# Kernel optimization log

Measured on AMD Instinct MI355X. Metric: run time of the kernel, lower is better.

The kernel has to match this reference:

```python
import jax, jax.numpy as jnp
import numpy as np

SEQ_LEN = 8192
D_MODEL = 1024
D_K = 128
D_V = 128


def setup_inputs() -> dict:
    key = jax.random.key(0)
    kx, kq, kk, kv = jax.random.split(key, 4)
    # xavier-uniform scale for (out, in) linear weights
    def xavier(k, out_f, in_f):
        lim = np.sqrt(6.0 / (in_f + out_f))
        return jax.random.uniform(k, (out_f, in_f), jnp.float32, -lim, lim)
    return {
        "X": jax.random.normal(kx, (SEQ_LEN, D_MODEL), jnp.float32),
        "Wq": xavier(kq, D_K, D_MODEL),
        "Wk": xavier(kk, D_K, D_MODEL),
        "Wv": xavier(kv, D_V, D_MODEL),
    }


def reference(X, Wq, Wk, Wv):
    # X: (S, d_model); W*: (d_k, d_model) torch Linear weights (y = x @ W.T)
    S = X.shape[0]
    Q = X @ Wq.T                      # (S, d_k)
    K = X @ Wk.T                      # (S, d_k)
    V = X @ Wv.T                      # (S, d_v)
    scale = jnp.sqrt(jnp.asarray(D_K, X.dtype))
    scores = (Q @ K.T) / scale        # (S, S)
    causal = jnp.tril(jnp.ones((S, S), bool))
    scores = jnp.where(causal, scores, -jnp.inf)
    weights = jax.nn.softmax(scores, axis=1)
    # dropout p=0.0 -> identity
    Z = weights @ V                   # (S, d_v)
    return Z
```

## Files before the change

### kernel.cpp

```cpp
#include <hip/hip_runtime.h>
#include <hip/hip_bf16.h>

#define S_LEN 8192
#define DM    1024
#define DK    128
#define KSTR  136
#define VSTR  72
#define SLOTD 2112
#define NCMAX 16

typedef __attribute__((ext_vector_type(8))) short bf16x8;
typedef __attribute__((ext_vector_type(8))) _Float16 f16x8;
typedef __attribute__((ext_vector_type(4))) float f32x4;
typedef __attribute__((ext_vector_type(16))) float f32x16;

__device__ __forceinline__ f32x4 mfma16(bf16x8 a, bf16x8 b, f32x4 c) {
    return __builtin_amdgcn_mfma_f32_16x16x32_bf16(a, b, c, 0, 0, 0);
}
__device__ __forceinline__ f32x16 mfma32(bf16x8 a, bf16x8 b, f32x16 c) {
    return __builtin_amdgcn_mfma_f32_32x32x16_bf16(a, b, c, 0, 0, 0);
}

__device__ __forceinline__ ushort f2bf(float f) {
    unsigned u = __builtin_bit_cast(unsigned, f);
    u += 0x7FFFu + ((u >> 16) & 1u);
    return (ushort)(u >> 16);
}

__device__ __forceinline__ ushort f2h(float f) {
    return __builtin_bit_cast(ushort, (_Float16)f);
}

__device__ __forceinline__ uint cvt_pk_bf16(float a, float b) {
    uint r;
    asm("v_cvt_pk_bf16_f32 %0, %1, %2" : "=v"(r) : "v"(a), "v"(b));
    return r;
}

__global__ __launch_bounds__(256, 1)
void convert_kernel(const float* __restrict__ X,
                    const float* __restrict__ Wq,
                    const float* __restrict__ Wk,
                    const float* __restrict__ Wv,
                    _Float16* __restrict__ Xh,
                    _Float16* __restrict__ Wh) {
    const int NX4 = S_LEN * DM / 4;
    const int NW4 = DK * DM / 4;
    const int total4 = NX4 + 3 * NW4;
    for (int i = blockIdx.x * 256 + threadIdx.x; i < total4; i += gridDim.x * 256) {
        const float4* src;
        _Float16* dst;
        int off;
        if (i < NX4) {
            src = (const float4*)X; dst = Xh; off = i;
        } else {
            const int w = i - NX4;
            const int which = w / NW4;
            off = w - which * NW4;
            src = (const float4*)(which == 0 ? Wq : (which == 1 ? Wk : Wv));
            dst = Wh + which * (DK * DM);
        }
        const float4 v = src[off];
        union { _Float16 h[4]; uint2 u; } p;
        p.h[0] = (_Float16)v.x; p.h[1] = (_Float16)v.y;
        p.h[2] = (_Float16)v.z; p.h[3] = (_Float16)v.w;
        *(uint2*)(dst + (size_t)off * 4) = p.u;
    }
}

__global__ __launch_bounds__(256)
void proj_gemm_kernel(const _Float16* __restrict__ Xh,
                      const _Float16* __restrict__ Wh,
                      ushort* __restrict__ Qb,
                      ushort* __restrict__ Kb,
                      ushort* __restrict__ Vtb) {
    __shared__ _Float16 Ash[32 * 32];
    __shared__ _Float16 Bsh[128 * 32];

    const int tid  = threadIdx.x;
    const int lane = tid & 63;
    const int quad = lane >> 4;
    const int l15  = lane & 15;
    const int wv   = tid >> 6;
    const int wm   = wv & 1;
    const int wn   = wv >> 1;
    const int m0   = blockIdx.x * 32;
    const int nb   = blockIdx.y;
    const _Float16* Wbase = Wh + nb * (DK * DM);

    f32x4 acc[4];
#pragma unroll
    for (int ni = 0; ni < 4; ++ni) acc[ni] = (f32x4){0.f, 0.f, 0.f, 0.f};

    for (int kk = 0; kk < DM; kk += 32) {
        __syncthreads();
        for (int s = tid; s < 640; s += 256) {
            if (s < 128) {
                const int row = s >> 2, sg = s & 3;
                __builtin_amdgcn_global_load_lds(
                    (const __attribute__((address_space(1))) void*)(Xh + (size_t)(m0 + row) * DM + kk + sg * 8),
                    (__attribute__((address_space(3))) void*)(Ash + s * 8), 16, 0, 0);
            } else {
                const int t = s - 128;
                const int row = t >> 2, sg = t & 3;
                __builtin_amdgcn_global_load_lds(
                    (const __attribute__((address_space(1))) void*)(Wbase + (size_t)row * DM + kk + sg * 8),
                    (__attribute__((address_space(3))) void*)(Bsh + t * 8), 16, 0, 0);
            }
        }
        __syncthreads();

        const f16x8 af = *(const f16x8*)(Ash + (wm * 16 + l15) * 32 + quad * 8);
        f16x8 bf[4];
#pragma unroll
        for (int t = 0; t < 4; ++t)
            bf[t] = *(const f16x8*)(Bsh + (wn * 64 + t * 16 + l15) * 32 + quad * 8);
#pragma unroll
        for (int ni = 0; ni < 4; ++ni)
            acc[ni] = __builtin_amdgcn_mfma_f32_16x16x32_f16(af, bf[ni], acc[ni], 0, 0, 0);
    }

    if (nb == 2) {
#pragma unroll
        for (int ni = 0; ni < 4; ++ni) {
            const int n = wn * 64 + ni * 16 + l15;
            const int m = m0 + wm * 16 + quad * 4;
            union { ushort h[4]; uint2 u; } p;
#pragma unroll
            for (int r = 0; r < 4; ++r) p.h[r] = f2bf(acc[ni][r]);
            *(uint2*)(Vtb + (size_t)n * S_LEN + m) = p.u;
        }
    } else {
        ushort* Ob = (nb == 0) ? Qb : Kb;
        const float sc = (nb == 0) ? 0.088388347648318447f * 1.4426950408889634f : 1.0f;
#pragma unroll
        for (int ni = 0; ni < 4; ++ni) {
            const int n = wn * 64 + ni * 16 + l15;
#pragma unroll
            for (int r = 0; r < 4; ++r) {
                const int m = m0 + wm * 16 + quad * 4 + r;
                Ob[(size_t)m * DK + n] = f2bf(acc[ni][r] * sc);
            }
        }
    }
}

__global__ __launch_bounds__(256, 2)
void flash_partial_kernel(const ushort* __restrict__ Qg,
                          const ushort* __restrict__ Kg,
                          const ushort* __restrict__ Vtg,
                          float* __restrict__ Part) {
    __shared__ __align__(16) ushort Ks [2][64 * KSTR];
    __shared__ __align__(16) ushort Vts[2][128 * VSTR];

    int rem = 543 - (int)blockIdx.x;
    int qb = 0;
    for (;;) {
        const int nc = (2 * qb + 9) >> 3;
        if (rem < nc) break;
        rem -= nc; ++qb;
    }
    const int NC    = (2 * qb + 9) >> 3;
    const int chunk = rem;
    const int nkt   = 2 * qb + 2;
    const int kt_lo = chunk * nkt / NC;
    const int kt_hi = (chunk + 1) * nkt / NC;

    const int tid  = threadIdx.x;
    const int wv   = tid >> 6;
    const int lane = tid & 63;
    const int l31  = lane & 31;
    const int hi   = lane >> 5;
    const int q0w  = qb * 128 + wv * 32;
    const int qrow = q0w + l31;

    bf16x8 qf[8];
    {
        const ushort* qp = Qg + (size_t)qrow * DK + hi * 8;
#pragma unroll
        for (int i = 0; i < 8; ++i) qf[i] = *(const bf16x8*)(qp + i * 16);
    }

    float m_ = -__builtin_inff();
    float l_ = 0.f;
    f32x16 acc[4];
#pragma unroll
    for (int dt = 0; dt < 4; ++dt)
#pragma unroll
        for (int j = 0; j < 16; ++j) acc[dt][j] = 0.f;

    bf16x8 stg[8];
#define LOAD_TILE(K0)                                                          \
    {                                                                          \
        const int k0_ = (K0);                                                  \
        _Pragma("unroll")                                                      \
        for (int i = 0; i < 8; ++i) {                                          \
            const int c = tid + (i << 8);                                      \
            if (c < 1024) {                                                    \
                const int row = c >> 4, ch = c & 15;                           \
                stg[i] = *(const bf16x8*)(Kg + (size_t)(k0_ + row) * DK + ch * 8); \
            } else {                                                           \
                const int cc = c - 1024;                                       \
                const int row = cc >> 3, ch = cc & 7;                          \
                stg[i] = *(const bf16x8*)(Vtg + (size_t)row * S_LEN + k0_ + ch * 8); \
            }                                                                  \
        }                                                                      \
    }
#define WRITE_BUF(B)                                                           \
    {                                                                          \
        ushort* Kb_ = Ks[B]; ushort* Vb_ = Vts[B];                             \
        _Pragma("unroll")                                                      \
        for (int i = 0; i < 8; ++i) {                                          \
            const int c = tid + (i << 8);                                      \
            if (c < 1024) {                                                    \
                const int row = c >> 4, ch = c & 15;                           \
                *(bf16x8*)(Kb_ + row * KSTR + ch * 8) = stg[i];                \
            } else {                                                           \
                const int cc = c - 1024;                                       \
                const int row = cc >> 3, ch = cc & 7;                          \
                const int s_lo = ((ch & 1) << 2) + (((ch >> 1) & 1) << 4) + ((ch >> 2) << 5); \
                union { bf16x8 v; uint2 q2[2]; } u;                            \
                u.v = stg[i];                                                  \
                ushort* vb = Vb_ + row * VSTR + s_lo;                          \
                *(uint2*)vb       = u.q2[0];                                   \
                *(uint2*)(vb + 8) = u.q2[1];                                   \
            }                                                                  \
        }                                                                      \
    }

    LOAD_TILE(kt_lo * 64)
    WRITE_BUF(0)
    if (kt_lo + 1 < kt_hi) LOAD_TILE((kt_lo + 1) * 64)
    __syncthreads();

    for (int kt = kt_lo; kt < kt_hi; ++kt) {
        const int k0 = kt * 64;
        const int cb = (kt - kt_lo) & 1;
        const ushort* ks = Ks[cb];
        const ushort* vs = Vts[cb];
        const bool prc = (k0 <= q0w);

        f32x16 Sr0, Sr1;
        if (prc) {
            __builtin_amdgcn_s_setprio(1);
#pragma unroll
            for (int j = 0; j < 16; ++j) { Sr0[j] = 0.f; Sr1[j] = 0.f; }
            const ushort* ka0 = ks + l31 * KSTR + hi * 8;
            const ushort* ka1 = ka0 + 32 * KSTR;
#pragma unroll
            for (int i = 0; i < 8; ++i)
                Sr0 = mfma32(*(const bf16x8*)(ka0 + i * 16), qf[i], Sr0);
#pragma unroll
            for (int i = 0; i < 8; ++i)
                Sr1 = mfma32(*(const bf16x8*)(ka1 + i * 16), qf[i], Sr1);
            __builtin_amdgcn_s_setprio(0);
        }

        if (kt + 1 < kt_hi) {
            WRITE_BUF(cb ^ 1)
            if (kt + 2 < kt_hi) LOAD_TILE((kt + 2) * 64)
        }

        if (prc) {
            if (k0 + 63 > q0w) {
#pragma unroll
                for (int r = 0; r < 16; ++r) {
                    const int krow = (r & 3) + 8 * (r >> 2) + 4 * hi;
                    if (k0 + krow > qrow)      Sr0[r] = -__builtin_inff();
                    if (k0 + 32 + krow > qrow) Sr1[r] = -__builtin_inff();
                }
            }

            float pmax = Sr0[0];
#pragma unroll
            for (int r = 1; r < 16; ++r) pmax = fmaxf(pmax, Sr0[r]);
#pragma unroll
            for (int r = 0; r < 16; ++r) pmax = fmaxf(pmax, Sr1[r]);
            pmax = fmaxf(pmax, __shfl_xor(pmax, 32));
            if (__any(pmax > m_ + 8.f)) {
                const float mnew = fmaxf(m_, pmax);
                const float al = __builtin_amdgcn_exp2f(m_ - mnew);
                m_ = mnew;
                l_ *= al;
#pragma unroll
                for (int dt = 0; dt < 4; ++dt)
#pragma unroll
                    for (int j = 0; j < 16; ++j) acc[dt][j] *= al;
            }
            float rs = 0.f;
            uint pfa[16];
            {
                float p0[16], p1[16];
#pragma unroll
                for (int r = 0; r < 16; ++r) { p0[r] = __builtin_amdgcn_exp2f(Sr0[r] - m_); rs += p0[r]; }
#pragma unroll
                for (int r = 0; r < 16; ++r) { p1[r] = __builtin_amdgcn_exp2f(Sr1[r] - m_); rs += p1[r]; }
#pragma unroll
                for (int j = 0; j < 4; ++j) {
                    pfa[j]      = cvt_pk_bf16(p0[2 * j],     p0[2 * j + 1]);
                    pfa[4 + j]  = cvt_pk_bf16(p0[8 + 2 * j], p0[8 + 2 * j + 1]);
                    pfa[8 + j]  = cvt_pk_bf16(p1[2 * j],     p1[2 * j + 1]);
                    pfa[12 + j] = cvt_pk_bf16(p1[8 + 2 * j], p1[8 + 2 * j + 1]);
                }
            }
            rs += __shfl_xor(rs, 32);
            l_ += rs;

            __builtin_amdgcn_s_setprio(1);
#pragma unroll
            for (int kc = 0; kc < 4; ++kc) {
                union { uint u[4]; bf16x8 v; } pu;
#pragma unroll
                for (int j = 0; j < 4; ++j) pu.u[j] = pfa[4 * kc + j];
                const ushort* va = vs + l31 * VSTR + kc * 16 + hi * 8;
#pragma unroll
                for (int dt = 0; dt < 4; ++dt)
                    acc[dt] = mfma32(*(const bf16x8*)(va + dt * 32 * VSTR), pu.v, acc[dt]);
            }
            __builtin_amdgcn_s_setprio(0);
        }
        __syncthreads();
    }
#undef LOAD_TILE
#undef WRITE_BUF

    const int qt32 = qb * 4 + wv;
    float* slot = Part + (size_t)(qt32 * NCMAX + chunk) * SLOTD;
    if (hi == 0) {
        slot[l31]      = m_;
        slot[32 + l31] = l_;
    }
    uint* slotO = (uint*)(slot + 64);
#pragma unroll
    for (int dt = 0; dt < 4; ++dt)
#pragma unroll
        for (int s = 0; s < 4; ++s) {
            uint2 w;
            w.x = (uint)f2h(acc[dt][4 * s])     | ((uint)f2h(acc[dt][4 * s + 1]) << 16);
            w.y = (uint)f2h(acc[dt][4 * s + 2]) | ((uint)f2h(acc[dt][4 * s + 3]) << 16);
            *(uint2*)(slotO + l31 * 64 + dt * 16 + s * 4 + hi * 2) = w;
        }
}

__global__ __launch_bounds__(256)
void flash_merge_kernel(const float* __restrict__ Part, float* __restrict__ Out) {
    __shared__ float Ms[32], Ls[32];
    __shared__ float Sc[16][32];
    const int qt = blockIdx.x;
    const int qb = qt >> 2;
    const int P  = (2 * qb + 9) >> 3;
    const int q0 = qt * 32;
    const int tid = threadIdx.x;
    const float* base = Part + (size_t)qt * NCMAX * SLOTD;

    if (tid < 32) {
        float M = -__builtin_inff();
        for (int p = 0; p < P; ++p) M = fmaxf(M, base[p * SLOTD + tid]);
        float L = 0.f;
        for (int p = 0; p < P; ++p)
            L += base[p * SLOTD + 32 + tid] * exp2f(base[p * SLOTD + tid] - M);
        Ms[tid] = M; Ls[tid] = L;
    }
    __syncthreads();
    for (int j = tid; j < 512; j += 256) {
        const int p = j >> 5, row = j & 31;
        Sc[p][row] = (p < P) ? exp2f(base[p * SLOTD + row] - Ms[row]) : 0.f;
    }
    __syncthreads();

#pragma unroll
    for (int j = tid; j < 2048; j += 256) {
        const int row = j >> 6, c2 = j & 63;
        float o0 = 0.f, o1 = 0.f;
        for (int p = 0; p < P; ++p) {
            const uint u = ((const uint*)(base + p * SLOTD + 64))[row * 64 + c2];
            const float sc = Sc[p][row];
            o0 += (float)__builtin_bit_cast(_Float16, (ushort)(u & 0xFFFF)) * sc;
            o1 += (float)__builtin_bit_cast(_Float16, (ushort)(u >> 16)) * sc;
        }
        const float inv = 1.0f / Ls[row];
        float2 o; o.x = o0 * inv; o.y = o1 * inv;
        *(float2*)(Out + (size_t)(q0 + row) * DK + c2 * 2) = o;
    }
}

extern "C" void kernel_launch(void* const* d_in, const int* in_sizes, int n_in,
                              void* d_out, int out_size, void* d_ws, size_t ws_size,
                              hipStream_t stream) {
    const float* X  = (const float*)d_in[0];
    const float* Wq = (const float*)d_in[1];
    const float* Wk = (const float*)d_in[2];
    const float* Wv = (const float*)d_in[3];
    ushort* ws  = (ushort*)d_ws;
    ushort* Qb  = ws;
    ushort* Kb  = ws + (size_t)S_LEN * DK;
    ushort* Vtb = ws + 2 * (size_t)S_LEN * DK;
    _Float16* Xh = (_Float16*)(ws + 3 * (size_t)S_LEN * DK);
    _Float16* Wh = Xh + (size_t)S_LEN * DM;
    float* Part = (float*)Xh;
    float* Out = (float*)d_out;

    convert_kernel<<<1024, 256, 0, stream>>>(X, Wq, Wk, Wv, Xh, Wh);
    proj_gemm_kernel<<<dim3(256, 3), 256, 0, stream>>>(Xh, Wh, Qb, Kb, Vtb);
    flash_partial_kernel<<<544, 256, 0, stream>>>(Qb, Kb, Vtb, Part);
    flash_merge_kernel<<<256, 256, 0, stream>>>(Part, Out);
}
```

Measured before the change: 171.0 us.

## Fuse X fp16 conversion into projection GEMM, double-buffer, split merge

Drops the separate X-to-fp16 conversion pass: the projection GEMM now loads fp32 X rows straight into registers and converts them while staging to LDS. This removes a full write and read of the fp16 X copy. Each block now computes all three projections for 16 rows, with double-buffered LDS tiles so the next tile's loads overlap the current MFMAs. The merge kernel is split across two blocks per query tile to raise parallelism. The trade-off is more redundant W traffic per block, a larger LDS footprint and a smaller M tile.

After: 169.4 us. About the same (-1.0%).

```diff
diff --git a/kernel.cpp b/kernel.cpp
--- a/kernel.cpp
+++ b/kernel.cpp
@@ -14,8 +14,8 @@
 typedef __attribute__((ext_vector_type(4))) float f32x4;
 typedef __attribute__((ext_vector_type(16))) float f32x16;
 
-__device__ __forceinline__ f32x4 mfma16(bf16x8 a, bf16x8 b, f32x4 c) {
-    return __builtin_amdgcn_mfma_f32_16x16x32_bf16(a, b, c, 0, 0, 0);
+__device__ __forceinline__ f32x4 mfma16f(f16x8 a, f16x8 b, f32x4 c) {
+    return __builtin_amdgcn_mfma_f32_16x16x32_f16(a, b, c, 0, 0, 0);
 }
 __device__ __forceinline__ f32x16 mfma32(bf16x8 a, bf16x8 b, f32x16 c) {
     return __builtin_amdgcn_mfma_f32_32x32x16_bf16(a, b, c, 0, 0, 0);
@@ -38,110 +38,115 @@
 }
 
 __global__ __launch_bounds__(256, 1)
-void convert_kernel(const float* __restrict__ X,
-                    const float* __restrict__ Wq,
-                    const float* __restrict__ Wk,
-                    const float* __restrict__ Wv,
-                    _Float16* __restrict__ Xh,
-                    _Float16* __restrict__ Wh) {
-    const int NX4 = S_LEN * DM / 4;
+void convert_w_kernel(const float* __restrict__ Wq,
+                      const float* __restrict__ Wk,
+                      const float* __restrict__ Wv,
+                      _Float16* __restrict__ Wh) {
     const int NW4 = DK * DM / 4;
-    const int total4 = NX4 + 3 * NW4;
-    for (int i = blockIdx.x * 256 + threadIdx.x; i < total4; i += gridDim.x * 256) {
-        const float4* src;
-        _Float16* dst;
-        int off;
-        if (i < NX4) {
-            src = (const float4*)X; dst = Xh; off = i;
-        } else {
-            const int w = i - NX4;
-            const int which = w / NW4;
-            off = w - which * NW4;
-            src = (const float4*)(which == 0 ? Wq : (which == 1 ? Wk : Wv));
-            dst = Wh + which * (DK * DM);
-        }
-        const float4 v = src[off];
-        union { _Float16 h[4]; uint2 u; } p;
-        p.h[0] = (_Float16)v.x; p.h[1] = (_Float16)v.y;
-        p.h[2] = (_Float16)v.z; p.h[3] = (_Float16)v.w;
-        *(uint2*)(dst + (size_t)off * 4) = p.u;
-    }
+    const int i = blockIdx.x * 256 + threadIdx.x;
+    const int which = i / NW4;
+    const int off = i - which * NW4;
+    const float4 v = ((const float4*)(which == 0 ? Wq : (which == 1 ? Wk : Wv)))[off];
+    union { _Float16 h[4]; uint2 u; } p;
+    p.h[0] = (_Float16)v.x; p.h[1] = (_Float16)v.y;
+    p.h[2] = (_Float16)v.z; p.h[3] = (_Float16)v.w;
+    *(uint2*)(Wh + (size_t)which * (DK * DM) + (size_t)off * 4) = p.u;
 }
 
 __global__ __launch_bounds__(256)
-void proj_gemm_kernel(const _Float16* __restrict__ Xh,
+void proj_gemm_kernel(const float* __restrict__ X,
                       const _Float16* __restrict__ Wh,
                       ushort* __restrict__ Qb,
                       ushort* __restrict__ Kb,
                       ushort* __restrict__ Vtb) {
-    __shared__ _Float16 Ash[32 * 32];
-    __shared__ _Float16 Bsh[128 * 32];
+    __shared__ _Float16 Ash[2][16 * 32];
+    __shared__ _Float16 Bsh[2][384 * 32];
 
     const int tid  = threadIdx.x;
     const int lane = tid & 63;
     const int quad = lane >> 4;
     const int l15  = lane & 15;
     const int wv   = tid >> 6;
-    const int wm   = wv & 1;
-    const int wn   = wv >> 1;
-    const int m0   = blockIdx.x * 32;
-    const int nb   = blockIdx.y;
-    const _Float16* Wbase = Wh + nb * (DK * DM);
-
-    f32x4 acc[4];
-#pragma unroll
-    for (int ni = 0; ni < 4; ++ni) acc[ni] = (f32x4){0.f, 0.f, 0.f, 0.f};
-
-    for (int kk = 0; kk < DM; kk += 32) {
+    const int m0   = blockIdx.x * 16;
+    const int arow = tid >> 3, ac4 = tid & 7;
+
+    f32x4 acc[3][2];
+#pragma unroll
+    for (int nb = 0; nb < 3; ++nb)
+#pragma unroll
+        for (int ni = 0; ni < 2; ++ni) acc[nb][ni] = (f32x4){0.f, 0.f, 0.f, 0.f};
+
+#define STAGE_B(KK, BUF)                                                       \
+    {                                                                          \
+        _Pragma("unroll")                                                      \
+        for (int s_ = tid; s_ < 1536; s_ += 256) {                             \
+            const int row_ = s_ >> 2, sg_ = s_ & 3;                            \
+            __builtin_amdgcn_global_load_lds(                                  \
+                (const __attribute__((address_space(1))) void*)(Wh + (size_t)row_ * DM + (KK) + sg_ * 8), \
+                (__attribute__((address_space(3))) void*)(Bsh[BUF] + s_ * 8), 16, 0, 0); \
+        }                                                                      \
+    }
+#define LOAD_A(DST, KK)                                                        \
+    if (tid < 128) (DST) = *(const float4*)(X + (size_t)(m0 + arow) * DM + (KK) + ac4 * 4);
+#define WRITE_A(SRC, BUF)                                                      \
+    if (tid < 128) {                                                           \
+        union { _Float16 h[4]; uint2 u; } pa_;                                 \
+        pa_.h[0] = (_Float16)(SRC).x; pa_.h[1] = (_Float16)(SRC).y;            \
+        pa_.h[2] = (_Float16)(SRC).z; pa_.h[3] = (_Float16)(SRC).w;            \
+        *(uint2*)(Ash[BUF] + arow * 32 + ac4 * 4) = pa_.u;                     \
+    }
+#define COMPUTE(BUF)                                                           \
+    {                                                                          \
+        const f16x8 af_ = *(const f16x8*)(Ash[BUF] + l15 * 32 + quad * 8);     \
+        _Pragma("unroll")                                                      \
+        for (int nb_ = 0; nb_ < 3; ++nb_)                                      \
+            _Pragma("unroll")                                                  \
+            for (int ni_ = 0; ni_ < 2; ++ni_) {                                \
+                const f16x8 bf_ = *(const f16x8*)(Bsh[BUF] + (nb_ * 128 + wv * 32 + ni_ * 16 + l15) * 32 + quad * 8); \
+                acc[nb_][ni_] = mfma16f(af_, bf_, acc[nb_][ni_]);              \
+            }                                                                  \
+    }
+
+    float4 ra, rb;
+    LOAD_A(ra, 0)
+    LOAD_A(rb, 32)
+    STAGE_B(0, 0)
+    WRITE_A(ra, 0)
+    __syncthreads();
+
+    for (int kk = 0; kk < DM; kk += 64) {
+        if (kk + 32 < DM) STAGE_B(kk + 32, 1)
+        if (kk + 64 < DM) LOAD_A(ra, kk + 64)
+        COMPUTE(0)
+        if (kk + 32 < DM) WRITE_A(rb, 1)
         __syncthreads();
-        for (int s = tid; s < 640; s += 256) {
-            if (s < 128) {
-                const int row = s >> 2, sg = s & 3;
-                __builtin_amdgcn_global_load_lds(
-                    (const __attribute__((address_space(1))) void*)(Xh + (size_t)(m0 + row) * DM + kk + sg * 8),
-                    (__attribute__((address_space(3))) void*)(Ash + s * 8), 16, 0, 0);
-            } else {
-                const int t = s - 128;
-                const int row = t >> 2, sg = t & 3;
-                __builtin_amdgcn_global_load_lds(
-                    (const __attribute__((address_space(1))) void*)(Wbase + (size_t)row * DM + kk + sg * 8),
-                    (__attribute__((address_space(3))) void*)(Bsh + t * 8), 16, 0, 0);
-            }
-        }
-        __syncthreads();
-
-        const f16x8 af = *(const f16x8*)(Ash + (wm * 16 + l15) * 32 + quad * 8);
-        f16x8 bf[4];
-#pragma unroll
-        for (int t = 0; t < 4; ++t)
-            bf[t] = *(const f16x8*)(Bsh + (wn * 64 + t * 16 + l15) * 32 + quad * 8);
-#pragma unroll
-        for (int ni = 0; ni < 4; ++ni)
-            acc[ni] = __builtin_amdgcn_mfma_f32_16x16x32_f16(af, bf[ni], acc[ni], 0, 0, 0);
-    }
-
-    if (nb == 2) {
-#pragma unroll
-        for (int ni = 0; ni < 4; ++ni) {
-            const int n = wn * 64 + ni * 16 + l15;
-            const int m = m0 + wm * 16 + quad * 4;
-            union { ushort h[4]; uint2 u; } p;
-#pragma unroll
-            for (int r = 0; r < 4; ++r) p.h[r] = f2bf(acc[ni][r]);
-            *(uint2*)(Vtb + (size_t)n * S_LEN + m) = p.u;
-        }
-    } else {
-        ushort* Ob = (nb == 0) ? Qb : Kb;
-        const float sc = (nb == 0) ? 0.088388347648318447f * 1.4426950408889634f : 1.0f;
-#pragma unroll
-        for (int ni = 0; ni < 4; ++ni) {
-            const int n = wn * 64 + ni * 16 + l15;
-#pragma unroll
-            for (int r = 0; r < 4; ++r) {
-                const int m = m0 + wm * 16 + quad * 4 + r;
-                Ob[(size_t)m * DK + n] = f2bf(acc[ni][r] * sc);
-            }
-        }
+        if (kk + 32 < DM) {
+            if (kk + 64 < DM) STAGE_B(kk + 64, 0)
+            if (kk + 96 < DM) LOAD_A(rb, kk + 96)
+            COMPUTE(1)
+            if (kk + 64 < DM) WRITE_A(ra, 0)
+            __syncthreads();
+        }
+    }
+#undef STAGE_B
+#undef LOAD_A
+#undef WRITE_A
+#undef COMPUTE
+
+    const float scq = 0.088388347648318447f * 1.4426950408889634f;
+#pragma unroll
+    for (int ni = 0; ni < 2; ++ni) {
+        const int n = wv * 32 + ni * 16 + l15;
+#pragma unroll
+        for (int r = 0; r < 4; ++r)
+            Qb[(size_t)(m0 + quad * 4 + r) * DK + n] = f2bf(acc[0][ni][r] * scq);
+#pragma unroll
+        for (int r = 0; r < 4; ++r)
+            Kb[(size_t)(m0 + quad * 4 + r) * DK + n] = f2bf(acc[1][ni][r]);
+        union { ushort h[4]; uint2 u; } p;
+#pragma unroll
+        for (int r = 0; r < 4; ++r) p.h[r] = f2bf(acc[2][ni][r]);
+        *(uint2*)(Vtb + (size_t)n * S_LEN + m0 + quad * 4) = p.u;
     }
 }
 
@@ -346,7 +351,8 @@
 void flash_merge_kernel(const float* __restrict__ Part, float* __restrict__ Out) {
     __shared__ float Ms[32], Ls[32];
     __shared__ float Sc[16][32];
-    const int qt = blockIdx.x;
+    const int qt   = blockIdx.x >> 1;
+    const int half = blockIdx.x & 1;
     const int qb = qt >> 2;
     const int P  = (2 * qb + 9) >> 3;
     const int q0 = qt * 32;
@@ -369,8 +375,8 @@
     __syncthreads();
 
 #pragma unroll
-    for (int j = tid; j < 2048; j += 256) {
-        const int row = j >> 6, c2 = j & 63;
+    for (int j = tid; j < 1024; j += 256) {
+        const int row = j >> 5, c2 = (j & 31) + half * 32;
         float o0 = 0.f, o1 = 0.f;
         for (int p = 0; p < P; ++p) {
             const uint u = ((const uint*)(base + p * SLOTD + 64))[row * 64 + c2];
@@ -395,13 +401,12 @@
     ushort* Qb  = ws;
     ushort* Kb  = ws + (size_t)S_LEN * DK;
     ushort* Vtb = ws + 2 * (size_t)S_LEN * DK;
-    _Float16* Xh = (_Float16*)(ws + 3 * (size_t)S_LEN * DK);
-    _Float16* Wh = Xh + (size_t)S_LEN * DM;
-    float* Part = (float*)Xh;
+    _Float16* Wh = (_Float16*)(ws + 3 * (size_t)S_LEN * DK);
+    float* Part = (float*)(Wh + (size_t)3 * DK * DM);
     float* Out = (float*)d_out;
 
-    convert_kernel<<<1024, 256, 0, stream>>>(X, Wq, Wk, Wv, Xh, Wh);
-    proj_gemm_kernel<<<dim3(256, 3), 256, 0, stream>>>(Xh, Wh, Qb, Kb, Vtb);
+    convert_w_kernel<<<384, 256, 0, stream>>>(Wq, Wk, Wv, Wh);
+    proj_gemm_kernel<<<512, 256, 0, stream>>>(X, Wh, Qb, Kb, Vtb);
     flash_partial_kernel<<<544, 256, 0, stream>>>(Qb, Kb, Vtb, Part);
-    flash_merge_kernel<<<256, 256, 0, stream>>>(Part, Out);
-}
+    flash_merge_kernel<<<512, 256, 0, stream>>>(Part, Out);
+}
```
